# Kernel optimization log

Hardware: AMD Instinct MI355X
Metric: run time of the kernel (lower is better)

## Reference

```python
import jax, jax.numpy as jnp
import numpy as np

N, C, H, W, P = 64, 256, 64, 64, 1024
GAMMA = 1.0  # __init__ arg


def setup_inputs() -> dict:
    key = jax.random.key(0)
    k1, k2, k3 = jax.random.split(key, 3)
    inp = jax.random.normal(k1, (N, C, H, W), dtype=jnp.float32)
    # absolute pixel coords (y, x) in [0, H-1] x [0, W-1]
    point = jax.random.uniform(k2, (N, P, 2), dtype=jnp.float32) * jnp.array([H - 1, W - 1], dtype=jnp.float32)
    offset = jax.random.normal(k3, (N, P, 2), dtype=jnp.float32) * 0.5
    return {"input": inp, "point": point, "offset": offset}


def _bilinear_sample(inp, pos):
    """inp: [n,c,h,w]; pos: [n,p,2] (y,x) absolute pixel coords -> [n,p,c].
    Out-of-bounds corners contribute zero (matches CUDA bilinear with zero padding)."""
    n, c, h, w = inp.shape
    y = pos[..., 0]
    x = pos[..., 1]
    y0f = jnp.floor(y)
    x0f = jnp.floor(x)
    ly = y - y0f  # fractional parts
    lx = x - x0f
    hy = 1.0 - ly
    hx = 1.0 - lx
    y0 = y0f.astype(jnp.int32)
    x0 = x0f.astype(jnp.int32)

    feat = jnp.transpose(inp, (0, 2, 3, 1))  # [n,h,w,c] for contiguous channel gather
    b = jnp.arange(n)[:, None]  # [n,1] broadcast against [n,p]

    def gather(yi, xi):
        valid = (yi >= 0) & (yi < h) & (xi >= 0) & (xi < w)  # [n,p]
        yc = jnp.clip(yi, 0, h - 1)
        xc = jnp.clip(xi, 0, w - 1)
        v = feat[b, yc, xc]  # [n,p,c]
        return v * valid[..., None].astype(v.dtype)

    v00 = gather(y0, x0)
    v01 = gather(y0, x0 + 1)
    v10 = gather(y0 + 1, x0)
    v11 = gather(y0 + 1, x0 + 1)

    w00 = (hy * hx)[..., None]
    w01 = (hy * lx)[..., None]
    w10 = (ly * hx)[..., None]
    w11 = (ly * lx)[..., None]
    return v00 * w00 + v01 * w01 + v10 * w10 + v11 * w11


def reference(input, point, offset):
    pos = point + GAMMA * offset  # [n,p,2] (y,x)
    return _bilinear_sample(input, pos)
```

## Files before the change

kernel.cpp:

```cpp
#include <hip/hip_runtime.h>

constexpr int N = 64, C = 256, H = 64, W = 64, P = 1024;
constexpr int PLANE   = H * W;
constexpr int GC      = 8;
constexpr int THREADS = 256;
constexpr int PPT     = 4;
constexpr int NBUF    = 3;

typedef float v4f __attribute__((ext_vector_type(4)));

__device__ __forceinline__ void stage_plane(const float* __restrict__ src,
                                            float* __restrict__ dst, int t) {
    const int tb = t & ~63;
    #pragma unroll
    for (int i = 0; i < 4; ++i) {
        const int j  = (i << 8) + t;
        const int jb = (i << 8) + tb;
        __builtin_amdgcn_global_load_lds(
            (const __attribute__((address_space(1))) void*)(src + (j << 2)),
            (__attribute__((address_space(3))) void*)(dst + (jb << 2)),
            16, 0, 0);
    }
}

__global__ __launch_bounds__(THREADS) void progressive_sample_kernel(
    const float* __restrict__ inp,
    const float* __restrict__ point,
    const float* __restrict__ offset,
    float* __restrict__ out)
{
    __shared__ __align__(16) float buf[NBUF][PLANE];

    const int b = blockIdx.x;
    const int n = b >> 5;
    const int g = b & 31;
    const int t = threadIdx.x;
    const int chan0 = g * GC;

    const float* src = inp + ((size_t)n * C + chan0) * PLANE;

    float2 pt_[PPT], of_[PPT];
    #pragma unroll
    for (int i = 0; i < PPT; ++i) {
        const int p = (i << 8) + t;
        pt_[i] = ((const float2*)point )[((size_t)n << 10) + p];
        of_[i] = ((const float2*)offset)[((size_t)n << 10) + p];
    }
    stage_plane(src,          buf[0], t);
    stage_plane(src + PLANE,  buf[1], t);

    int   i00[PPT], i01[PPT], i10[PPT], i11[PPT];
    float w00[PPT], w01[PPT], w10[PPT], w11[PPT];
    #pragma unroll
    for (int i = 0; i < PPT; ++i) {
        const float y = pt_[i].x + of_[i].x;
        const float x = pt_[i].y + of_[i].y;
        const float y0f = floorf(y), x0f = floorf(x);
        const float ly = y - y0f, lx = x - x0f;
        const float hy = 1.0f - ly, hx = 1.0f - lx;
        const int y0 = (int)y0f, x0 = (int)x0f, y1 = y0 + 1, x1 = x0 + 1;
        const bool vy0 = (unsigned)y0 < (unsigned)H, vy1 = (unsigned)y1 < (unsigned)H;
        const bool vx0 = (unsigned)x0 < (unsigned)W, vx1 = (unsigned)x1 < (unsigned)W;
        const int yc0 = min(max(y0, 0), H - 1), yc1 = min(max(y1, 0), H - 1);
        const int xc0 = min(max(x0, 0), W - 1), xc1 = min(max(x1, 0), W - 1);
        i00[i] = yc0 * W + xc0; i01[i] = yc0 * W + xc1;
        i10[i] = yc1 * W + xc0; i11[i] = yc1 * W + xc1;
        w00[i] = (vy0 && vx0) ? hy * hx : 0.0f;
        w01[i] = (vy0 && vx1) ? hy * lx : 0.0f;
        w10[i] = (vy1 && vx0) ? ly * hx : 0.0f;
        w11[i] = (vy1 && vx1) ? ly * lx : 0.0f;
    }

    float acc[PPT][GC];

    #pragma unroll
    for (int k = 0; k < GC; ++k) {
        if (k < GC - 1) {
            asm volatile("s_waitcnt vmcnt(4)" ::: "memory");
        } else {
            asm volatile("s_waitcnt vmcnt(0)" ::: "memory");
        }
        __builtin_amdgcn_sched_barrier(0);
        __builtin_amdgcn_s_barrier();
        __builtin_amdgcn_sched_barrier(0);

        if (k + 2 < GC)
            stage_plane(src + (size_t)(k + 2) * PLANE, buf[(k + 2) % NBUF], t);

        const float* __restrict__ bk = buf[k % NBUF];
        #pragma unroll
        for (int i = 0; i < PPT; ++i) {
            acc[i][k] = bk[i00[i]] * w00[i] + bk[i01[i]] * w01[i]
                      + bk[i10[i]] * w10[i] + bk[i11[i]] * w11[i];
        }

        asm volatile("s_waitcnt lgkmcnt(0)" ::: "memory");
        __builtin_amdgcn_sched_barrier(0);
    }

    #pragma unroll
    for (int i = 0; i < PPT; ++i) {
        float* o = out + (((size_t)n << 10) + ((i << 8) + t)) * C + chan0;
        v4f v0 = { acc[i][0], acc[i][1], acc[i][2], acc[i][3] };
        v4f v1 = { acc[i][4], acc[i][5], acc[i][6], acc[i][7] };
        *(v4f*)o       = v0;
        *(v4f*)(o + 4) = v1;
    }
}

extern "C" void kernel_launch(void* const* d_in, const int* in_sizes, int n_in,
                              void* d_out, int out_size, void* d_ws, size_t ws_size,
                              hipStream_t stream) {
    const float* inp    = (const float*)d_in[0];
    const float* point  = (const float*)d_in[1];
    const float* offset = (const float*)d_in[2];
    float* out = (float*)d_out;

    progressive_sample_kernel<<<N * (C / GC), THREADS, 0, stream>>>(
        inp, point, offset, out);
}
```

Before: 82.19 us.

## Use 1024-thread blocks with one point per thread and deeper LDS pipeline

Each block now runs 1024 threads, so every thread handles one sample point instead of four, and each thread stages one 16-byte chunk per plane. The LDS ring grows from three to four plane buffers with prefetch distance three, and the vmcnt waits are adjusted to match. The aim is more waves in flight to hide LDS gather and global load latency. In exchange, LDS per block rises to 64KB and every barrier now synchronises 16 waves, which may limit how many blocks fit per CU.

```diff
diff --git a/kernel.cpp b/kernel.cpp
--- a/kernel.cpp
+++ b/kernel.cpp
@@ -3,27 +3,21 @@
 constexpr int N = 64, C = 256, H = 64, W = 64, P = 1024;
 constexpr int PLANE   = H * W;
 constexpr int GC      = 8;
-constexpr int THREADS = 256;
-constexpr int PPT     = 4;
-constexpr int NBUF    = 3;
+constexpr int THREADS = 1024;
+constexpr int NBUF    = 4;
 
 typedef float v4f __attribute__((ext_vector_type(4)));
 
 __device__ __forceinline__ void stage_plane(const float* __restrict__ src,
                                             float* __restrict__ dst, int t) {
     const int tb = t & ~63;
-    #pragma unroll
-    for (int i = 0; i < 4; ++i) {
-        const int j  = (i << 8) + t;
-        const int jb = (i << 8) + tb;
-        __builtin_amdgcn_global_load_lds(
-            (const __attribute__((address_space(1))) void*)(src + (j << 2)),
-            (__attribute__((address_space(3))) void*)(dst + (jb << 2)),
-            16, 0, 0);
-    }
+    __builtin_amdgcn_global_load_lds(
+        (const __attribute__((address_space(1))) void*)(src + (t << 2)),
+        (__attribute__((address_space(3))) void*)(dst + (tb << 2)),
+        16, 0, 0);
 }
 
-__global__ __launch_bounds__(THREADS) void progressive_sample_kernel(
+__global__ __launch_bounds__(THREADS, 2) void progressive_sample_kernel(
     const float* __restrict__ inp,
     const float* __restrict__ point,
     const float* __restrict__ offset,
@@ -39,44 +33,37 @@
 
     const float* src = inp + ((size_t)n * C + chan0) * PLANE;
 
-    float2 pt_[PPT], of_[PPT];
-    #pragma unroll
-    for (int i = 0; i < PPT; ++i) {
-        const int p = (i << 8) + t;
-        pt_[i] = ((const float2*)point )[((size_t)n << 10) + p];
-        of_[i] = ((const float2*)offset)[((size_t)n << 10) + p];
-    }
-    stage_plane(src,          buf[0], t);
-    stage_plane(src + PLANE,  buf[1], t);
+    const float2 pt2 = ((const float2*)point )[((size_t)n << 10) + t];
+    const float2 of2 = ((const float2*)offset)[((size_t)n << 10) + t];
+    stage_plane(src,             buf[0], t);
+    stage_plane(src + PLANE,     buf[1], t);
+    stage_plane(src + 2 * PLANE, buf[2], t);
 
-    int   i00[PPT], i01[PPT], i10[PPT], i11[PPT];
-    float w00[PPT], w01[PPT], w10[PPT], w11[PPT];
-    #pragma unroll
-    for (int i = 0; i < PPT; ++i) {
-        const float y = pt_[i].x + of_[i].x;
-        const float x = pt_[i].y + of_[i].y;
-        const float y0f = floorf(y), x0f = floorf(x);
-        const float ly = y - y0f, lx = x - x0f;
-        const float hy = 1.0f - ly, hx = 1.0f - lx;
-        const int y0 = (int)y0f, x0 = (int)x0f, y1 = y0 + 1, x1 = x0 + 1;
-        const bool vy0 = (unsigned)y0 < (unsigned)H, vy1 = (unsigned)y1 < (unsigned)H;
-        const bool vx0 = (unsigned)x0 < (unsigned)W, vx1 = (unsigned)x1 < (unsigned)W;
-        const int yc0 = min(max(y0, 0), H - 1), yc1 = min(max(y1, 0), H - 1);
-        const int xc0 = min(max(x0, 0), W - 1), xc1 = min(max(x1, 0), W - 1);
-        i00[i] = yc0 * W + xc0; i01[i] = yc0 * W + xc1;
-        i10[i] = yc1 * W + xc0; i11[i] = yc1 * W + xc1;
-        w00[i] = (vy0 && vx0) ? hy * hx : 0.0f;
-        w01[i] = (vy0 && vx1) ? hy * lx : 0.0f;
-        w10[i] = (vy1 && vx0) ? ly * hx : 0.0f;
-        w11[i] = (vy1 && vx1) ? ly * lx : 0.0f;
-    }
+    const float y = pt2.x + of2.x;
+    const float x = pt2.y + of2.y;
+    const float y0f = floorf(y), x0f = floorf(x);
+    const float ly = y - y0f, lx = x - x0f;
+    const float hy = 1.0f - ly, hx = 1.0f - lx;
+    const int y0 = (int)y0f, x0 = (int)x0f, y1 = y0 + 1, x1 = x0 + 1;
+    const bool vy0 = (unsigned)y0 < (unsigned)H, vy1 = (unsigned)y1 < (unsigned)H;
+    const bool vx0 = (unsigned)x0 < (unsigned)W, vx1 = (unsigned)x1 < (unsigned)W;
+    const int yc0 = min(max(y0, 0), H - 1), yc1 = min(max(y1, 0), H - 1);
+    const int xc0 = min(max(x0, 0), W - 1), xc1 = min(max(x1, 0), W - 1);
+    const int i00 = yc0 * W + xc0, i01 = yc0 * W + xc1;
+    const int i10 = yc1 * W + xc0, i11 = yc1 * W + xc1;
+    const float w00 = (vy0 && vx0) ? hy * hx : 0.0f;
+    const float w01 = (vy0 && vx1) ? hy * lx : 0.0f;
+    const float w10 = (vy1 && vx0) ? ly * hx : 0.0f;
+    const float w11 = (vy1 && vx1) ? ly * lx : 0.0f;
 
-    float acc[PPT][GC];
+    float acc[GC];
 
     #pragma unroll
     for (int k = 0; k < GC; ++k) {
-        if (k < GC - 1) {
-            asm volatile("s_waitcnt vmcnt(4)" ::: "memory");
+        if (k <= GC - 3) {
+            asm volatile("s_waitcnt vmcnt(2)" ::: "memory");
+        } else if (k == GC - 2) {
+            asm volatile("s_waitcnt vmcnt(1)" ::: "memory");
         } else {
             asm volatile("s_waitcnt vmcnt(0)" ::: "memory");
         }
@@ -84,28 +71,22 @@
         __builtin_amdgcn_s_barrier();
         __builtin_amdgcn_sched_barrier(0);
 
-        if (k + 2 < GC)
-            stage_plane(src + (size_t)(k + 2) * PLANE, buf[(k + 2) % NBUF], t);
+        if (k + 3 < GC)
+            stage_plane(src + (size_t)(k + 3) * PLANE, buf[(k + 3) & 3], t);
 
-        const float* __restrict__ bk = buf[k % NBUF];
-        #pragma unroll
-        for (int i = 0; i < PPT; ++i) {
-            acc[i][k] = bk[i00[i]] * w00[i] + bk[i01[i]] * w01[i]
-                      + bk[i10[i]] * w10[i] + bk[i11[i]] * w11[i];
-        }
+        const float* __restrict__ bk = buf[k & 3];
+        acc[k] = bk[i00] * w00 + bk[i01] * w01
+               + bk[i10] * w10 + bk[i11] * w11;
 
         asm volatile("s_waitcnt lgkmcnt(0)" ::: "memory");
         __builtin_amdgcn_sched_barrier(0);
     }
 
-    #pragma unroll
-    for (int i = 0; i < PPT; ++i) {
-        float* o = out + (((size_t)n << 10) + ((i << 8) + t)) * C + chan0;
-        v4f v0 = { acc[i][0], acc[i][1], acc[i][2], acc[i][3] };
-        v4f v1 = { acc[i][4], acc[i][5], acc[i][6], acc[i][7] };
-        *(v4f*)o       = v0;
-        *(v4f*)(o + 4) = v1;
-    }
+    float* o = out + (((size_t)n << 10) + t) * C + chan0;
+    v4f v0 = { acc[0], acc[1], acc[2], acc[3] };
+    v4f v1 = { acc[4], acc[5], acc[6], acc[7] };
+    *(v4f*)o       = v0;
+    *(v4f*)(o + 4) = v1;
 }
 
 extern "C" void kernel_launch(void* const* d_in, const int* in_sizes, int n_in,
```

Result: faster. 79.32 us (-3.5%).
